# Performance work log

Hardware: AMD Instinct MI355X
Metric: run time of the kernel (lower is better)

Reference implementation:

```python
import jax, jax.numpy as jnp
import numpy as np

B, S, N, D = 8, 2048, 4, 1024  # batch, seq, residual streams, model dim


def setup_inputs() -> dict:
    key = jax.random.key(0)
    k1, k2, k3, k4 = jax.random.split(key, 4)
    return {
        "x": jax.random.normal(k1, (B, S, N, D), dtype=jnp.float32),
        "h_res": jax.random.normal(k2, (B, S, N, N), dtype=jnp.float32),
        "h_out": jax.random.normal(k3, (B, S, D), dtype=jnp.float32),
        "h_post": jax.random.normal(k4, (B, S, N), dtype=jnp.float32),
    }


def reference(x, h_res, h_out, h_post):
    # Batched per-sample small GEMM over the stream dim: [.., n, n] @ [.., n, D]
    mixed = jnp.einsum("bsij,bsjd->bsid", h_res, x)
    # Fused epilogue: scale the GEMM result by h_out (per model-dim) and
    # combine with the h_post-scaled residual streams.
    # (The NPU kernel's n/D padding is layout-only: zero pad then slice back.)
    return mixed * h_out[:, :, None, :] + h_post[..., None] * x
```

## Files before the change

### kernel.cpp

```cpp
#include <hip/hip_runtime.h>


#define NB 8
#define NS 2048
#define NN 4
#define ND 1024

typedef float v4f __attribute__((ext_vector_type(4)));

__global__ __launch_bounds__(256) void fused_stream_mix(
    const float* __restrict__ x,
    const float* __restrict__ h_res,
    const float* __restrict__ h_out,
    const float* __restrict__ h_post,
    float* __restrict__ out)
{
    const int bs = blockIdx.x;
    const int t  = threadIdx.x;

    const v4f* __restrict__ xp = (const v4f*)(x + (size_t)bs * NN * ND);
    const v4f x0 = __builtin_nontemporal_load(xp + 0 * (ND / 4) + t);
    const v4f x1 = __builtin_nontemporal_load(xp + 1 * (ND / 4) + t);
    const v4f x2 = __builtin_nontemporal_load(xp + 2 * (ND / 4) + t);
    const v4f x3 = __builtin_nontemporal_load(xp + 3 * (ND / 4) + t);
    const v4f ho = __builtin_nontemporal_load(
        (const v4f*)(h_out + (size_t)bs * ND) + t);

    const float* __restrict__ hr = h_res  + (size_t)bs * (NN * NN);
    const float* __restrict__ hq = h_post + (size_t)bs * NN;
    float r[NN * NN];
    float p[NN];
    #pragma unroll
    for (int k = 0; k < NN * NN; ++k) r[k] = hr[k];
    #pragma unroll
    for (int i = 0; i < NN; ++i) p[i] = hq[i];

    v4f* __restrict__ op = (v4f*)(out + (size_t)bs * NN * ND);

    #pragma unroll
    for (int i = 0; i < NN; ++i) {
        const float r0 = r[i * NN + 0];
        const float r1 = r[i * NN + 1];
        const float r2 = r[i * NN + 2];
        const float r3 = r[i * NN + 3];
        const float hp = p[i];
        const v4f xi = (i == 0) ? x0 : (i == 1) ? x1 : (i == 2) ? x2 : x3;

        v4f m;
        m.x = (r0 * x0.x + r1 * x1.x + r2 * x2.x + r3 * x3.x) * ho.x + hp * xi.x;
        m.y = (r0 * x0.y + r1 * x1.y + r2 * x2.y + r3 * x3.y) * ho.y + hp * xi.y;
        m.z = (r0 * x0.z + r1 * x1.z + r2 * x2.z + r3 * x3.z) * ho.z + hp * xi.z;
        m.w = (r0 * x0.w + r1 * x1.w + r2 * x2.w + r3 * x3.w) * ho.w + hp * xi.w;

        __builtin_nontemporal_store(m, op + i * (ND / 4) + t);
    }
}

extern "C" void kernel_launch(void* const* d_in, const int* in_sizes, int n_in,
                              void* d_out, int out_size, void* d_ws, size_t ws_size,
                              hipStream_t stream) {
    const float* x      = (const float*)d_in[0];
    const float* h_res  = (const float*)d_in[1];
    const float* h_out  = (const float*)d_in[2];
    const float* h_post = (const float*)d_in[3];
    float* out = (float*)d_out;

    fused_stream_mix<<<NB * NS, 256, 0, stream>>>(x, h_res, h_out, h_post, out);
}
```

Measured before the change: 455.5 us.

## Use persistent grid with register double-buffered prefetch of next row

Launches a fixed grid of 1024 blocks, each looping over 16 (batch, seq) rows and prefetching the next row's inputs into registers while computing and storing the current one. h_res and h_post are now loaded as float4 vectors instead of scalars. The aim is to hide memory latency and cut per-block launch overhead. In exchange it lowers the number of resident waves and doubles register usage, which may reduce memory-level parallelism.

```diff
diff --git a/kernel.cpp b/kernel.cpp
--- a/kernel.cpp
+++ b/kernel.cpp
@@ -5,54 +5,76 @@
 #define NS 2048
 #define NN 4
 #define ND 1024
+#define GRID 1024
+#define ITER ((NB * NS) / GRID)
 
 typedef float v4f __attribute__((ext_vector_type(4)));
 
-__global__ __launch_bounds__(256) void fused_stream_mix(
+struct Streams {
+    v4f x0, x1, x2, x3;
+    v4f ho;
+    v4f r0, r1, r2, r3;
+    v4f p;
+};
+
+__device__ __forceinline__ void load_bs(int bs, int t,
+                                        const float* __restrict__ x,
+                                        const float* __restrict__ h_res,
+                                        const float* __restrict__ h_out,
+                                        const float* __restrict__ h_post,
+                                        Streams& s)
+{
+    const v4f* __restrict__ xp = (const v4f*)(x + (size_t)bs * NN * ND);
+    s.x0 = __builtin_nontemporal_load(xp + 0 * (ND / 4) + t);
+    s.x1 = __builtin_nontemporal_load(xp + 1 * (ND / 4) + t);
+    s.x2 = __builtin_nontemporal_load(xp + 2 * (ND / 4) + t);
+    s.x3 = __builtin_nontemporal_load(xp + 3 * (ND / 4) + t);
+    s.ho = __builtin_nontemporal_load((const v4f*)(h_out + (size_t)bs * ND) + t);
+    const v4f* __restrict__ hr = (const v4f*)(h_res + (size_t)bs * (NN * NN));
+    s.r0 = hr[0]; s.r1 = hr[1]; s.r2 = hr[2]; s.r3 = hr[3];
+    s.p  = *(const v4f*)(h_post + (size_t)bs * NN);
+}
+
+__device__ __forceinline__ void compute_store(int bs, int t, const Streams& s,
+                                              float* __restrict__ out)
+{
+    v4f* __restrict__ op = (v4f*)(out + (size_t)bs * NN * ND);
+    #pragma unroll
+    for (int i = 0; i < NN; ++i) {
+        const v4f rr = (i == 0) ? s.r0 : (i == 1) ? s.r1 : (i == 2) ? s.r2 : s.r3;
+        const v4f xi = (i == 0) ? s.x0 : (i == 1) ? s.x1 : (i == 2) ? s.x2 : s.x3;
+        const float hp = s.p[i];
+
+        v4f m;
+        m.x = (rr.x * s.x0.x + rr.y * s.x1.x + rr.z * s.x2.x + rr.w * s.x3.x) * s.ho.x + hp * xi.x;
+        m.y = (rr.x * s.x0.y + rr.y * s.x1.y + rr.z * s.x2.y + rr.w * s.x3.y) * s.ho.y + hp * xi.y;
+        m.z = (rr.x * s.x0.z + rr.y * s.x1.z + rr.z * s.x2.z + rr.w * s.x3.z) * s.ho.z + hp * xi.z;
+        m.w = (rr.x * s.x0.w + rr.y * s.x1.w + rr.z * s.x2.w + rr.w * s.x3.w) * s.ho.w + hp * xi.w;
+
+        __builtin_nontemporal_store(m, op + i * (ND / 4) + t);
+    }
+}
+
+__global__ __launch_bounds__(256, 4) void fused_stream_mix(
     const float* __restrict__ x,
     const float* __restrict__ h_res,
     const float* __restrict__ h_out,
     const float* __restrict__ h_post,
     float* __restrict__ out)
 {
-    const int bs = blockIdx.x;
-    const int t  = threadIdx.x;
+    const int b = blockIdx.x;
+    const int t = threadIdx.x;
 
-    const v4f* __restrict__ xp = (const v4f*)(x + (size_t)bs * NN * ND);
-    const v4f x0 = __builtin_nontemporal_load(xp + 0 * (ND / 4) + t);
-    const v4f x1 = __builtin_nontemporal_load(xp + 1 * (ND / 4) + t);
-    const v4f x2 = __builtin_nontemporal_load(xp + 2 * (ND / 4) + t);
-    const v4f x3 = __builtin_nontemporal_load(xp + 3 * (ND / 4) + t);
-    const v4f ho = __builtin_nontemporal_load(
-        (const v4f*)(h_out + (size_t)bs * ND) + t);
-
-    const float* __restrict__ hr = h_res  + (size_t)bs * (NN * NN);
-    const float* __restrict__ hq = h_post + (size_t)bs * NN;
-    float r[NN * NN];
-    float p[NN];
-    #pragma unroll
-    for (int k = 0; k < NN * NN; ++k) r[k] = hr[k];
-    #pragma unroll
-    for (int i = 0; i < NN; ++i) p[i] = hq[i];
-
-    v4f* __restrict__ op = (v4f*)(out + (size_t)bs * NN * ND);
+    Streams cur, nxt;
+    load_bs(b, t, x, h_res, h_out, h_post, cur);
 
     #pragma unroll
-    for (int i = 0; i < NN; ++i) {
-        const float r0 = r[i * NN + 0];
-        const float r1 = r[i * NN + 1];
-        const float r2 = r[i * NN + 2];
-        const float r3 = r[i * NN + 3];
-        const float hp = p[i];
-        const v4f xi = (i == 0) ? x0 : (i == 1) ? x1 : (i == 2) ? x2 : x3;
-
-        v4f m;
-        m.x = (r0 * x0.x + r1 * x1.x + r2 * x2.x + r3 * x3.x) * ho.x + hp * xi.x;
-        m.y = (r0 * x0.y + r1 * x1.y + r2 * x2.y + r3 * x3.y) * ho.y + hp * xi.y;
-        m.z = (r0 * x0.z + r1 * x1.z + r2 * x2.z + r3 * x3.z) * ho.z + hp * xi.z;
-        m.w = (r0 * x0.w + r1 * x1.w + r2 * x2.w + r3 * x3.w) * ho.w + hp * xi.w;
-
-        __builtin_nontemporal_store(m, op + i * (ND / 4) + t);
+    for (int k = 0; k < ITER; ++k) {
+        if (k + 1 < ITER)
+            load_bs(b + (k + 1) * GRID, t, x, h_res, h_out, h_post, nxt);
+        compute_store(b + k * GRID, t, cur, out);
+        if (k + 1 < ITER)
+            cur = nxt;
     }
 }
 
@@ -65,5 +87,5 @@
     const float* h_post = (const float*)d_in[3];
     float* out = (float*)d_out;
 
-    fused_stream_mix<<<NB * NS, 256, 0, stream>>>(x, h_res, h_out, h_post, out);
+    fused_stream_mix<<<GRID, 256, 0, stream>>>(x, h_res, h_out, h_post, out);
 }
```

Result: no change. 455.1 us (-0.1%).
